# Optimization experiments

Measured on AMD Instinct MI355X. Metric: run time of the kernel, lower is better.

Reference implementation:

```python
import jax, jax.numpy as jnp
import numpy as np

NEG = -1e9


def _siglu(x):
    return x * jax.nn.sigmoid(x)


def setup_inputs() -> dict:
    key = jax.random.key(0)
    ks = jax.random.split(key, 10)
    B, S, M, D = 2, 2048, 64, 1024
    sc = 0.02
    return {
        "tokens": jax.random.normal(ks[0], (B, S, D), jnp.float32),
        "memory": jax.random.normal(ks[1], (B, M, D), jnp.float32),
        "Wq": jax.random.normal(ks[2], (D, D), jnp.float32) * sc,
        "bq": jnp.zeros((D,), jnp.float32),
        "Wk": jax.random.normal(ks[3], (D, D), jnp.float32) * sc,
        "bk": jnp.zeros((D,), jnp.float32),
        "Wv": jax.random.normal(ks[4], (D, D), jnp.float32) * sc,
        "bv": jnp.zeros((D,), jnp.float32),
        "Wo": jax.random.normal(ks[5], (D, D), jnp.float32) * sc,
        "bo": jnp.zeros((D,), jnp.float32),
        "pool_q": jax.random.normal(ks[6], (M, D), jnp.float32),
        "cell_W": jax.random.normal(ks[7], (2 * D, 2 * D), jnp.float32) * sc,
        "cell_b": jnp.zeros((2 * D,), jnp.float32),
    }


def reference(tokens, memory, Wq, bq, Wk, bk, Wv, bv, Wo, bo, pool_q, cell_W, cell_b):
    B, S, D = tokens.shape
    M = memory.shape[1]
    H = 16
    hd = D // H
    T = M + S

    x = jnp.concatenate([memory, tokens], axis=1)  # (B, T, D)

    # combined causal mask: memory rows/cols fully visible, token block causal
    tok_mask = jnp.triu(jnp.full((S, S), NEG, jnp.float32), k=1)
    mask = jnp.zeros((T, T), jnp.float32).at[M:, M:].set(tok_mask)  # (T, T)

    def heads(w, b):
        return (x @ w.T + b).reshape(B, T, H, hd).transpose(0, 2, 1, 3)

    q = heads(Wq, bq)  # (B, H, T, hd)
    k = heads(Wk, bk)
    v = heads(Wv, bv)

    scores = jnp.einsum("bhqd,bhkd->bhqk", q, k) * (hd ** -0.5) + mask
    attn = jax.nn.softmax(scores, axis=-1)
    ctx = jnp.einsum("bhqk,bhkd->bhqd", attn, v)
    ctx = ctx.transpose(0, 2, 1, 3).reshape(B, T, D)
    attn_out = ctx @ Wo.T + bo

    x = x + attn_out  # residual
    mem_out = x[:, :M]  # (B, M, D)
    tok_out = x[:, M:]  # (B, S, D)

    # attention pooling: one learnable query per memory slot
    pscores = jnp.einsum("md,bsd->bms", pool_q, tok_out) * (D ** -0.5)
    pweights = jax.nn.softmax(pscores, axis=-1)
    summary = jnp.einsum("bms,bsd->bmd", pweights, tok_out)  # (B, M, D)

    # MinimalRNNCell (siglu-gated) applied per memory slot
    combined = jnp.concatenate([mem_out, summary], axis=-1)  # (B, M, 2D)
    update = combined @ cell_W.T + cell_b
    gate, cand = jnp.split(update, 2, axis=-1)
    gate = jax.nn.sigmoid(gate)
    new_memory = mem_out * gate + (1.0 - gate) * _siglu(cand)

    return tok_out, new_memory
```

## Files before the change

### kernel.cpp

```cpp
#include <hip/hip_runtime.h>
#include <hip/hip_bf16.h>

#define B_  2
#define S_  2048
#define M_  64
#define D_  1024
#define T_  2112
#define H_  16
#define HD_ 64
#define BT_ (B_*T_)
#define NEGBIG (-1e9f)
#define LOG2E 1.44269504f

typedef float f32x4  __attribute__((ext_vector_type(4)));
typedef float f32x4b __attribute__((ext_vector_type(4)));
typedef short short8 __attribute__((ext_vector_type(8)));
typedef unsigned short u16x4 __attribute__((ext_vector_type(4)));
typedef __bf16 bf16x8 __attribute__((ext_vector_type(8)));

static __device__ __forceinline__ unsigned short bf16_of(float f) {
  __hip_bfloat16 h = __float2bfloat16(f);
  return __builtin_bit_cast(unsigned short, h);
}

static __device__ __forceinline__ f32x4 mfma_bf16(short8 a, short8 b, f32x4 c) {
  return __builtin_amdgcn_mfma_f32_16x16x32_bf16(
      __builtin_bit_cast(bf16x8, a), __builtin_bit_cast(bf16x8, b), c, 0, 0, 0);
}

static __device__ __forceinline__ void gload16(const void* g, void* lds) {
  __builtin_amdgcn_global_load_lds(
      (const __attribute__((address_space(1))) unsigned int*)g,
      (__attribute__((address_space(3))) unsigned int*)lds, 16, 0, 0);
}

static __device__ __forceinline__ short8 pack8(const float* v, float scale) {
  short8 o;
#pragma unroll
  for (int k = 0; k < 8; k++) o[k] = (short)bf16_of(v[k] * scale);
  return o;
}


__global__ void k_build_x(const float* __restrict__ tokens,
                          const float* __restrict__ memory,
                          unsigned short* __restrict__ xb) {
  const int NG = BT_ * D_ / 8;
  for (int gI = blockIdx.x * blockDim.x + threadIdx.x; gI < NG;
       gI += gridDim.x * blockDim.x) {
    int i = gI * 8;
    int b = (i >= T_ * D_) ? 1 : 0;
    int rem = i - b * (T_ * D_);
    int t = rem >> 10;
    int d = rem & 1023;
    const float* src = (t < M_) ? &memory[(((size_t)b * M_ + t) << 10) + d]
                                : &tokens[(((size_t)b * S_ + (t - M_)) << 10) + d];
    float v[8];
    *(f32x4*)&v[0] = *(const f32x4*)&src[0];
    *(f32x4*)&v[4] = *(const f32x4*)&src[4];
    *(short8*)&xb[i] = pack8(v, 1.f);
  }
}

__global__ void k_cast_all(const float* __restrict__ Wq, const float* __restrict__ Wk,
                           const float* __restrict__ Wv, const float* __restrict__ Wo,
                           const float* __restrict__ cW, const float* __restrict__ pq,
                           unsigned short* __restrict__ Wqkvb, unsigned short* __restrict__ Wob,
                           unsigned short* __restrict__ cWb, unsigned short* __restrict__ pqb) {
  const int NW = D_ * D_;
  const int NC = 4 * D_ * D_;
  const int NP = M_ * D_;
  const int NG = (4 * NW + NC + NP) / 8;
  for (int gI = blockIdx.x * blockDim.x + threadIdx.x; gI < NG;
       gI += gridDim.x * blockDim.x) {
    int i = gI * 8;
    const float* src;
    unsigned short* dst;
    float scale = 1.f;
    if (i < 3 * NW) {
      int which = i >> 20, j = i & (NW - 1);
      src = ((which == 0) ? Wq : (which == 1) ? Wk : Wv) + j;
      dst = Wqkvb + i;
    } else if (i < 4 * NW) {
      src = Wo + (i - 3 * NW);
      dst = Wob + (i - 3 * NW);
    } else if (i < 4 * NW + NC) {
      src = cW + (i - 4 * NW);
      dst = cWb + (i - 4 * NW);
    } else {
      src = pq + (i - 4 * NW - NC);
      dst = pqb + (i - 4 * NW - NC);
      scale = 0.03125f * LOG2E;
    }
    float v[8];
    *(f32x4*)&v[0] = *(const f32x4*)&src[0];
    *(f32x4*)&v[4] = *(const f32x4*)&src[4];
    *(short8*)dst = pack8(v, scale);
  }
}

__device__ __forceinline__ void gemm128_core(const unsigned short* __restrict__ A,
                                             const unsigned short* __restrict__ BT,
                                             int K, int m0, int n0,
                                             f32x4 acc[4][4]) {
  __shared__ __align__(16) unsigned short As[2][128][64];
  __shared__ __align__(16) unsigned short Bs[2][128][64];
  const int tid = threadIdx.x;
  const int w = tid >> 6, l = tid & 63;
  const int wr = w >> 1, wc = w & 1;
  const int lr = l & 15, lg = l >> 4;
  f32x4 z; z[0] = z[1] = z[2] = z[3] = 0.f;
#pragma unroll
  for (int i = 0; i < 4; i++)
#pragma unroll
    for (int j = 0; j < 4; j++) acc[i][j] = z;

  auto stage = [&](int buf, int k0) {
#pragma unroll
    for (int c = 0; c < 4; c++) {
      int rbase = c * 32 + w * 8;
      int rr = rbase + (l >> 3);
      int u = (l & 7) ^ (rr & 7);
      gload16(&A[(size_t)(m0 + rr) * K + k0 + u * 8], &As[buf][rbase][0]);
      gload16(&BT[(size_t)(n0 + rr) * K + k0 + u * 8], &Bs[buf][rbase][0]);
    }
  };

  stage(0, 0);
  int cur = 0;
  const int NK = K >> 6;
  for (int kt = 0; kt < NK; kt++) {
    if (kt + 1 < NK) {
      stage(cur ^ 1, (kt + 1) << 6);
      asm volatile("s_waitcnt vmcnt(8)" ::: "memory");
    } else {
      asm volatile("s_waitcnt vmcnt(0)" ::: "memory");
    }
    __builtin_amdgcn_s_barrier();

    short8 a[4][2], b[4][2];
#pragma unroll
    for (int i = 0; i < 4; i++) {
      int row = wr * 64 + i * 16 + lr;
      int sw = row & 7;
#pragma unroll
      for (int kk = 0; kk < 2; kk++)
        a[i][kk] = *(const short8*)&As[cur][row][(((kk << 2) | lg) ^ sw) * 8];
    }
#pragma unroll
    for (int j = 0; j < 4; j++) {
      int row = wc * 64 + j * 16 + lr;
      int sw = row & 7;
#pragma unroll
      for (int kk = 0; kk < 2; kk++)
        b[j][kk] = *(const short8*)&Bs[cur][row][(((kk << 2) | lg) ^ sw) * 8];
    }
    __builtin_amdgcn_s_setprio(1);
#pragma unroll
    for (int kk = 0; kk < 2; kk++)
#pragma unroll
      for (int i = 0; i < 4; i++)
#pragma unroll
        for (int j = 0; j < 4; j++)
          acc[i][j] = mfma_bf16(a[i][kk], b[j][kk], acc[i][j]);
    __builtin_amdgcn_s_setprio(0);

    __builtin_amdgcn_s_barrier();
    cur ^= 1;
  }
}

__device__ __forceinline__ void gemm_core(const unsigned short* __restrict__ A,
                                          const unsigned short* __restrict__ BT,
                                          int ldk, int Klen, int m0, int n0,
                                          f32x4 acc[4]) {
  __shared__ __align__(16) unsigned short As[64][40];
  __shared__ __align__(16) unsigned short Bs[64][40];
  const int tid = threadIdx.x;
  const int w = tid >> 6, l = tid & 63;
  const int sr = tid >> 2, sc = (tid & 3) * 8;
  f32x4 z; z[0] = z[1] = z[2] = z[3] = 0.f;
  acc[0] = acc[1] = acc[2] = acc[3] = z;
  for (int k0 = 0; k0 < Klen; k0 += 32) {
    __syncthreads();
    *(short8*)&As[sr][sc] = *(const short8*)&A[(size_t)(m0 + sr) * ldk + k0 + sc];
    *(short8*)&Bs[sr][sc] = *(const short8*)&BT[(size_t)(n0 + sr) * ldk + k0 + sc];
    __syncthreads();
    short8 a = *(const short8*)&As[w * 16 + (l & 15)][(l >> 4) * 8];
#pragma unroll
    for (int n = 0; n < 4; n++) {
      short8 b = *(const short8*)&Bs[n * 16 + (l & 15)][(l >> 4) * 8];
      acc[n] = mfma_bf16(a, b, acc[n]);
    }
  }
}

__global__ __launch_bounds__(256) void k_qkv(
    const unsigned short* __restrict__ xb, const unsigned short* __restrict__ Wqkvb,
    const float* __restrict__ bq, const float* __restrict__ bk,
    const float* __restrict__ bv, unsigned short* __restrict__ qg,
    unsigned short* __restrict__ kg, unsigned short* __restrict__ vTg) {
  const int id = blockIdx.x;
  const int xcd = id & 7;
  const int g = xcd * 99 + (id >> 3);
  const int mt = g / 24, nn = g - mt * 24;
  const int which = nn >> 3;
  const unsigned short* W = Wqkvb + (size_t)which * D_ * D_;
  const float* bias = (which == 0) ? bq : ((which == 1) ? bk : bv);
  f32x4 acc[4][4];
  const int m0 = mt * 128, n0 = (nn & 7) * 128;
  gemm128_core(xb, W, D_, m0, n0, acc);
  const int tid = threadIdx.x, w = tid >> 6, l = tid & 63;
  const int wr = w >> 1, wc = w & 1;
#pragma unroll
  for (int i = 0; i < 4; i++) {
#pragma unroll
    for (int j = 0; j < 4; j++) {
#pragma unroll
      for (int r = 0; r < 4; r++) {
        int m = m0 + wr * 64 + i * 16 + (l >> 4) * 4 + r;
        int c = n0 + wc * 64 + j * 16 + (l & 15);
        int b = (m >= T_) ? 1 : 0;
        int t = m - b * T_;
        int h = c >> 6, dh = c & 63;
        int bh = b * H_ + h;
        float v = acc[i][j][r] + bias[c];
        if (which == 0)
          qg[((size_t)bh * T_ + t) * HD_ + dh] = bf16_of(v * 0.125f * LOG2E);
        else if (which == 1)
          kg[((size_t)bh * T_ + t) * HD_ + dh] = bf16_of(v);
        else
          vTg[((size_t)bh * HD_ + dh) * T_ + t] = bf16_of(v);
      }
    }
  }
}

__global__ __launch_bounds__(256) void k_attn(
    const unsigned short* __restrict__ qg, const unsigned short* __restrict__ kg,
    const unsigned short* __restrict__ vTg, unsigned short* __restrict__ ctx) {
  const int id = blockIdx.x;
  const int xcd = id & 7;
  const int rem = id >> 3;
  const int g = rem / 33, qtr = rem - g * 33;
  const int qt = (qtr == 0) ? 0 : 33 - qtr;
  const int bh = g * 8 + xcd;
  const int tid = threadIdx.x, w = tid >> 6, l = tid & 63;
  const int lr = l & 15, lg = l >> 4;
  __shared__ __align__(16) unsigned short Ks[2][64][64];
  __shared__ __align__(16) unsigned short Vs[2][64][64];
  __shared__ __align__(16) unsigned short Ps[4][16][72];

  const unsigned short* qb = qg + (size_t)bh * T_ * HD_;
  const unsigned short* kb = kg + (size_t)bh * T_ * HD_;
  const unsigned short* vb = vTg + (size_t)bh * HD_ * T_;

  short8 aq[2];
  const int qrow = qt * 64 + w * 16 + lr;
#pragma unroll
  for (int st = 0; st < 2; st++)
    aq[st] = *(const short8*)&qb[(size_t)qrow * HD_ + st * 32 + lg * 8];

  f32x4 zz; zz[0] = zz[1] = zz[2] = zz[3] = 0.f;
  f32x4 o[4];
  o[0] = o[1] = o[2] = o[3] = zz;
  float mrun = -1e30f, lrun = 0.f;

  const int nkt = (qt == 0) ? 33 : qt + 1;

  auto stage = [&](int buf, int kb2) {
#pragma unroll
    for (int i = 0; i < 2; i++) {
      int rr = w * 16 + i * 8 + (l >> 3);
      int swz = ((l & 7) ^ (rr & 7)) * 8;
      gload16(&kb[(size_t)(kb2 + rr) * HD_ + swz], &Ks[buf][w * 16 + i * 8][0]);
      gload16(&vb[(size_t)rr * T_ + kb2 + swz], &Vs[buf][w * 16 + i * 8][0]);
    }
  };

  stage(0, 0);
  __syncthreads();
  int cur = 0;

  for (int j = 0; j < nkt; j++) {
    const int kbase = j * 64;
    if (j + 1 < nkt) stage(cur ^ 1, kbase + 64);

    short8 bkf[2][4];
#pragma unroll
    for (int n = 0; n < 4; n++) {
      int row = n * 16 + lr;
      int sw = lr & 7;
#pragma unroll
      for (int st = 0; st < 2; st++)
        bkf[st][n] = *(const short8*)&Ks[cur][row][((st * 4 + lg) ^ sw) * 8];
    }
    f32x4 s[4];
    s[0] = s[1] = s[2] = s[3] = zz;
    __builtin_amdgcn_s_setprio(1);
#pragma unroll
    for (int st = 0; st < 2; st++)
#pragma unroll
      for (int n = 0; n < 4; n++)
        s[n] = mfma_bf16(bkf[st][n], aq[st], s[n]);
    __builtin_amdgcn_s_setprio(0);

    if (qt > 0 && j == qt) {
      const int tql = w * 16 + lr;
#pragma unroll
      for (int n = 0; n < 4; n++)
#pragma unroll
        for (int r = 0; r < 4; r++) {
          int tkl = n * 16 + lg * 4 + r;
          if (tkl > tql) s[n][r] = NEGBIG;
        }
    }
    float pm = s[0][0];
#pragma unroll
    for (int n = 0; n < 4; n++)
#pragma unroll
      for (int r = 0; r < 4; r++) pm = fmaxf(pm, s[n][r]);
    pm = fmaxf(pm, __shfl_xor(pm, 16));
    pm = fmaxf(pm, __shfl_xor(pm, 32));

    if (__any(pm > mrun + 8.f)) {
      float mn = fmaxf(mrun, pm);
      float fac = exp2f(mrun - mn);
      mrun = mn;
      lrun *= fac;
      float fr[4];
#pragma unroll
      for (int r = 0; r < 4; r++) fr[r] = __shfl(fac, lg * 4 + r);
#pragma unroll
      for (int n = 0; n < 4; n++)
#pragma unroll
        for (int r = 0; r < 4; r++) o[n][r] *= fr[r];
    }
#pragma unroll
    for (int n = 0; n < 4; n++) {
      u16x4 pk;
#pragma unroll
      for (int r = 0; r < 4; r++) {
        float p = exp2f(s[n][r] - mrun);
        lrun += p;
        pk[r] = bf16_of(p);
      }
      *(u16x4*)&Ps[w][lr][n * 16 + lg * 4] = pk;
    }

    short8 bvf[2][4];
#pragma unroll
    for (int n = 0; n < 4; n++) {
      int row = n * 16 + lr;
      int sw = lr & 7;
#pragma unroll
      for (int st = 0; st < 2; st++)
        bvf[st][n] = *(const short8*)&Vs[cur][row][((st * 4 + lg) ^ sw) * 8];
    }
    short8 ap[2];
#pragma unroll
    for (int st = 0; st < 2; st++)
      ap[st] = *(const short8*)&Ps[w][lr][st * 32 + lg * 8];
    __builtin_amdgcn_s_setprio(1);
#pragma unroll
    for (int st = 0; st < 2; st++)
#pragma unroll
      for (int n = 0; n < 4; n++)
        o[n] = mfma_bf16(ap[st], bvf[st][n], o[n]);
    __builtin_amdgcn_s_setprio(0);

    __syncthreads();
    cur ^= 1;
  }
  lrun += __shfl_xor(lrun, 16);
  lrun += __shfl_xor(lrun, 32);
  float linv[4];
#pragma unroll
  for (int r = 0; r < 4; r++) linv[r] = 1.f / __shfl(lrun, lg * 4 + r);

  const int b = bh >> 4, h = bh & 15;
#pragma unroll
  for (int n = 0; n < 4; n++)
#pragma unroll
    for (int r = 0; r < 4; r++) {
      int tq = qt * 64 + w * 16 + lg * 4 + r;
      float val = o[n][r] * linv[r];
      ctx[((size_t)(b * T_ + tq)) * D_ + h * HD_ + n * 16 + lr] = bf16_of(val);
    }
}

__global__ __launch_bounds__(256) void k_out(
    const unsigned short* __restrict__ ctxb, const unsigned short* __restrict__ Wob,
    const float* __restrict__ bo, const float* __restrict__ tokens,
    const float* __restrict__ memory, float* __restrict__ out_tok,
    unsigned short* __restrict__ tokb, unsigned short* __restrict__ tokTb,
    float* __restrict__ memout, unsigned short* __restrict__ comb) {
  f32x4 acc[4][4];
  const int m0 = blockIdx.y * 128, n0 = blockIdx.x * 128;
  gemm128_core(ctxb, Wob, D_, m0, n0, acc);
  const int tid = threadIdx.x, w = tid >> 6, l = tid & 63;
  const int wr = w >> 1, wc = w & 1;
#pragma unroll
  for (int i = 0; i < 4; i++) {
#pragma unroll
    for (int j = 0; j < 4; j++) {
#pragma unroll
      for (int r = 0; r < 4; r++) {
        int m = m0 + wr * 64 + i * 16 + (l >> 4) * 4 + r;
        int c = n0 + wc * 64 + j * 16 + (l & 15);
        int b = (m >= T_) ? 1 : 0;
        int t = m - b * T_;
        float xo = (t < M_) ? memory[((size_t)b * M_ + t) * D_ + c]
                            : tokens[((size_t)b * S_ + (t - M_)) * D_ + c];
        float val = acc[i][j][r] + bo[c] + xo;
        if (t < M_) {
          memout[((size_t)b * M_ + t) * D_ + c] = val;
          comb[((size_t)b * M_ + t) * (2 * D_) + c] = bf16_of(val);
        } else {
          size_t ti = (size_t)b * S_ + (t - M_);
          out_tok[ti * D_ + c] = val;
          tokb[ti * D_ + c] = bf16_of(val);
          tokTb[((size_t)b * D_ + c) * S_ + (t - M_)] = bf16_of(val);
        }
      }
    }
  }
}

__global__ __launch_bounds__(256) void k_pscore_part(
    const unsigned short* __restrict__ pqb, const unsigned short* __restrict__ tokb,
    float* __restrict__ pscp) {
  const int stile = blockIdx.x, ks = blockIdx.y, b = blockIdx.z;
  f32x4 acc[4];
  gemm_core(pqb + ks * 256, tokb + (size_t)b * S_ * D_ + ks * 256, D_, 256,
            0, stile * 64, acc);
  const int tid = threadIdx.x, w = tid >> 6, l = tid & 63;
  float* dst = pscp + ((size_t)(ks * B_ + b) * M_) * S_;
#pragma unroll
  for (int n = 0; n < 4; n++) {
#pragma unroll
    for (int r = 0; r < 4; r++) {
      int m = w * 16 + (l >> 4) * 4 + r;
      int s = stile * 64 + n * 16 + (l & 15);
      dst[(size_t)m * S_ + s] = acc[n][r];
    }
  }
}

__global__ __launch_bounds__(256) void k_psoftmax(const float* __restrict__ pscp,
                                                  unsigned short* __restrict__ pw) {
  const int row = blockIdx.x;
  const int b = row >> 6, m = row & 63;
  const int tid = threadIdx.x;
  float v[8];
  float mx = -1e30f;
#pragma unroll
  for (int i = 0; i < 8; i++) {
    int s = tid + i * 256;
    float acc = 0.f;
#pragma unroll
    for (int ks = 0; ks < 4; ks++)
      acc += pscp[((size_t)(ks * B_ + b) * M_ + m) * S_ + s];
    v[i] = acc;
    mx = fmaxf(mx, acc);
  }
#pragma unroll
  for (int off = 1; off < 64; off <<= 1) mx = fmaxf(mx, __shfl_xor(mx, off));
  __shared__ float rm[4], rs[4];
  if ((tid & 63) == 0) rm[tid >> 6] = mx;
  __syncthreads();
  mx = fmaxf(fmaxf(rm[0], rm[1]), fmaxf(rm[2], rm[3]));
  float sum = 0.f;
#pragma unroll
  for (int i = 0; i < 8; i++) {
    v[i] = exp2f(v[i] - mx);
    sum += v[i];
  }
#pragma unroll
  for (int off = 1; off < 64; off <<= 1) sum += __shfl_xor(sum, off);
  if ((tid & 63) == 0) rs[tid >> 6] = sum;
  __syncthreads();
  float inv = 1.f / (rs[0] + rs[1] + rs[2] + rs[3]);
#pragma unroll
  for (int i = 0; i < 8; i++)
    pw[(size_t)row * S_ + tid + i * 256] = bf16_of(v[i] * inv);
}

__global__ __launch_bounds__(256) void k_summary_part(
    const unsigned short* __restrict__ pw, const unsigned short* __restrict__ tokTb,
    float* __restrict__ sump) {
  const int nt = blockIdx.x, ks = blockIdx.y, b = blockIdx.z;
  f32x4 acc[4];
  gemm_core(pw + (size_t)b * M_ * S_ + ks * 256,
            tokTb + (size_t)b * D_ * S_ + ks * 256, S_, 256, 0, nt * 64, acc);
  const int tid = threadIdx.x, w = tid >> 6, l = tid & 63;
  float* dst = sump + ((size_t)(ks * B_ + b) * M_) * D_;
#pragma unroll
  for (int n = 0; n < 4; n++) {
#pragma unroll
    for (int r = 0; r < 4; r++) {
      int m = w * 16 + (l >> 4) * 4 + r;
      int c = nt * 64 + n * 16 + (l & 15);
      dst[(size_t)m * D_ + c] = acc[n][r];
    }
  }
}

__global__ void k_sumcomb(const float* __restrict__ sump,
                          unsigned short* __restrict__ comb) {
  int i = blockIdx.x * blockDim.x + threadIdx.x;
  if (i >= B_ * M_ * D_) return;
  int bm = i >> 10, c = i & 1023;
  int b = bm >> 6, m = bm & 63;
  float acc = 0.f;
#pragma unroll
  for (int ks = 0; ks < 8; ks++)
    acc += sump[((size_t)(ks * B_ + b) * M_ + m) * D_ + c];
  comb[((size_t)b * M_ + m) * (2 * D_) + D_ + c] = bf16_of(acc);
}

__global__ __launch_bounds__(256) void k_cell_part(
    const unsigned short* __restrict__ comb, const unsigned short* __restrict__ cWb,
    float* __restrict__ cellp) {
  const int nt = blockIdx.x, mt = blockIdx.y, ks = blockIdx.z;
  f32x4 acc[4];
  gemm_core(comb + ks * 512, cWb + ks * 512, 2 * D_, 512, mt * 64, nt * 64, acc);
  const int tid = threadIdx.x, w = tid >> 6, l = tid & 63;
#pragma unroll
  for (int n = 0; n < 4; n++) {
#pragma unroll
    for (int r = 0; r < 4; r++) {
      int m = mt * 64 + w * 16 + (l >> 4) * 4 + r;
      int c = nt * 64 + n * 16 + (l & 15);
      cellp[((size_t)ks * (B_ * M_) + m) * (2 * D_) + c] = acc[n][r];
    }
  }
}

__global__ void k_newmem(const float* __restrict__ cellp,
                         const float* __restrict__ cb,
                         const float* __restrict__ memout,
                         float* __restrict__ out2) {
  int i = blockIdx.x * blockDim.x + threadIdx.x;
  if (i >= B_ * M_ * D_) return;
  int r = i >> 10, d = i & 1023;
  float gsum = cb[d], csum = cb[D_ + d];
#pragma unroll
  for (int ks = 0; ks < 4; ks++) {
    gsum += cellp[((size_t)ks * (B_ * M_) + r) * (2 * D_) + d];
    csum += cellp[((size_t)ks * (B_ * M_) + r) * (2 * D_) + D_ + d];
  }
  float sg = 1.f / (1.f + __expf(-gsum));
  float sc = 1.f / (1.f + __expf(-csum));
  out2[i] = memout[i] * sg + (1.f - sg) * (csum * sc);
}

extern "C" void kernel_launch(void* const* d_in, const int* in_sizes, int n_in,
                              void* d_out, int out_size, void* d_ws, size_t ws_size,
                              hipStream_t stream) {
  const float* tokens = (const float*)d_in[0];
  const float* memory = (const float*)d_in[1];
  const float* Wq = (const float*)d_in[2];
  const float* bq = (const float*)d_in[3];
  const float* Wk = (const float*)d_in[4];
  const float* bk = (const float*)d_in[5];
  const float* Wv = (const float*)d_in[6];
  const float* bv = (const float*)d_in[7];
  const float* Wo = (const float*)d_in[8];
  const float* bo = (const float*)d_in[9];
  const float* pool_q = (const float*)d_in[10];
  const float* cell_W = (const float*)d_in[11];
  const float* cell_b = (const float*)d_in[12];

  size_t off = 0;
  auto alloc = [&](size_t bytes) -> void* {
    void* p = (char*)d_ws + off;
    off += (bytes + 255) & ~(size_t)255;
    return p;
  };
  unsigned short* xb    = (unsigned short*)alloc((size_t)BT_ * D_ * 2);
  unsigned short* Wqkvb = (unsigned short*)alloc((size_t)3 * D_ * D_ * 2);
  unsigned short* Wob   = (unsigned short*)alloc((size_t)D_ * D_ * 2);
  unsigned short* cWb   = (unsigned short*)alloc((size_t)(2 * D_) * (2 * D_) * 2);
  unsigned short* pqb   = (unsigned short*)alloc((size_t)M_ * D_ * 2);
  unsigned short* qg    = (unsigned short*)alloc((size_t)B_ * H_ * T_ * HD_ * 2);
  unsigned short* kg    = (unsigned short*)alloc((size_t)B_ * H_ * T_ * HD_ * 2);
  unsigned short* vTg   = (unsigned short*)alloc((size_t)B_ * H_ * HD_ * T_ * 2);
  unsigned short* ctxb  = (unsigned short*)alloc((size_t)BT_ * D_ * 2);
  unsigned short* tokb  = (unsigned short*)alloc((size_t)B_ * S_ * D_ * 2);
  unsigned short* tokTb = (unsigned short*)alloc((size_t)B_ * D_ * S_ * 2);
  float*          memout= (float*)alloc((size_t)B_ * M_ * D_ * 4);
  unsigned short* comb  = (unsigned short*)alloc((size_t)B_ * M_ * 2 * D_ * 2);
  unsigned short* pwt   = (unsigned short*)alloc((size_t)B_ * M_ * S_ * 2);
  float*          pscp  = (float*)alloc((size_t)4 * B_ * M_ * S_ * 4);
  float*          sump  = (float*)alloc((size_t)8 * B_ * M_ * D_ * 4);
  float*          cellp = (float*)alloc((size_t)4 * B_ * M_ * 2 * D_ * 4);

  float* out_tok = (float*)d_out;
  float* out_mem = out_tok + (size_t)B_ * S_ * D_;

  k_build_x<<<2048, 256, 0, stream>>>(tokens, memory, xb);
  k_cast_all<<<2048, 256, 0, stream>>>(Wq, Wk, Wv, Wo, cell_W, pool_q,
                                       Wqkvb, Wob, cWb, pqb);

  k_qkv<<<792, 256, 0, stream>>>(xb, Wqkvb, bq, bk, bv, qg, kg, vTg);
  k_attn<<<1056, 256, 0, stream>>>(qg, kg, vTg, ctxb);
  k_out<<<dim3(8, 33), 256, 0, stream>>>(ctxb, Wob, bo, tokens, memory, out_tok,
                                         tokb, tokTb, memout, comb);
  k_pscore_part<<<dim3(32, 4, 2), 256, 0, stream>>>(pqb, tokb, pscp);
  k_psoftmax<<<B_ * M_, 256, 0, stream>>>(pscp, pwt);
  k_summary_part<<<dim3(16, 8, 2), 256, 0, stream>>>(pwt, tokTb, sump);
  k_sumcomb<<<512, 256, 0, stream>>>(sump, comb);
  k_cell_part<<<dim3(32, 2, 4), 256, 0, stream>>>(comb, cWb, cellp);
  k_newmem<<<512, 256, 0, stream>>>(cellp, cell_b, memout, out_mem);
}
```

Baseline: 220.6 us.

## Merge prep kernels, drop XCD block remap, halve split-K factors

Fuses the activation build and weight-cast kernels into one k_prep launch to save a launch and a tail. Replaces k_qkv's XCD-aware block index remapping with a plain 2D grid. Halves the split-K partition count for the pooling-score, summary and cell GEMMs, which reduces partial-sum traffic and reduction work but lowers parallelism for these small GEMMs.

New measurement: 235.7 us. 6.8% more time.

```diff
diff --git a/kernel.cpp b/kernel.cpp
--- a/kernel.cpp
+++ b/kernel.cpp
@@ -13,7 +13,6 @@
 #define LOG2E 1.44269504f
 
 typedef float f32x4  __attribute__((ext_vector_type(4)));
-typedef float f32x4b __attribute__((ext_vector_type(4)));
 typedef short short8 __attribute__((ext_vector_type(8)));
 typedef unsigned short u16x4 __attribute__((ext_vector_type(4)));
 typedef __bf16 bf16x8 __attribute__((ext_vector_type(8)));
@@ -41,56 +40,49 @@
   return o;
 }
 
-
-__global__ void k_build_x(const float* __restrict__ tokens,
-                          const float* __restrict__ memory,
-                          unsigned short* __restrict__ xb) {
-  const int NG = BT_ * D_ / 8;
-  for (int gI = blockIdx.x * blockDim.x + threadIdx.x; gI < NG;
-       gI += gridDim.x * blockDim.x) {
-    int i = gI * 8;
-    int b = (i >= T_ * D_) ? 1 : 0;
-    int rem = i - b * (T_ * D_);
-    int t = rem >> 10;
-    int d = rem & 1023;
-    const float* src = (t < M_) ? &memory[(((size_t)b * M_ + t) << 10) + d]
-                                : &tokens[(((size_t)b * S_ + (t - M_)) << 10) + d];
-    float v[8];
-    *(f32x4*)&v[0] = *(const f32x4*)&src[0];
-    *(f32x4*)&v[4] = *(const f32x4*)&src[4];
-    *(short8*)&xb[i] = pack8(v, 1.f);
-  }
-}
-
-__global__ void k_cast_all(const float* __restrict__ Wq, const float* __restrict__ Wk,
-                           const float* __restrict__ Wv, const float* __restrict__ Wo,
-                           const float* __restrict__ cW, const float* __restrict__ pq,
-                           unsigned short* __restrict__ Wqkvb, unsigned short* __restrict__ Wob,
-                           unsigned short* __restrict__ cWb, unsigned short* __restrict__ pqb) {
+__global__ void k_prep(const float* __restrict__ tokens, const float* __restrict__ memory,
+                       const float* __restrict__ Wq, const float* __restrict__ Wk,
+                       const float* __restrict__ Wv, const float* __restrict__ Wo,
+                       const float* __restrict__ cW, const float* __restrict__ pq,
+                       unsigned short* __restrict__ xb, unsigned short* __restrict__ Wqkvb,
+                       unsigned short* __restrict__ Wob, unsigned short* __restrict__ cWb,
+                       unsigned short* __restrict__ pqb) {
   const int NW = D_ * D_;
   const int NC = 4 * D_ * D_;
   const int NP = M_ * D_;
-  const int NG = (4 * NW + NC + NP) / 8;
+  const int NG1 = BT_ * D_ / 8;
+  const int NG = NG1 + (4 * NW + NC + NP) / 8;
   for (int gI = blockIdx.x * blockDim.x + threadIdx.x; gI < NG;
        gI += gridDim.x * blockDim.x) {
-    int i = gI * 8;
     const float* src;
     unsigned short* dst;
     float scale = 1.f;
-    if (i < 3 * NW) {
-      int which = i >> 20, j = i & (NW - 1);
-      src = ((which == 0) ? Wq : (which == 1) ? Wk : Wv) + j;
-      dst = Wqkvb + i;
-    } else if (i < 4 * NW) {
-      src = Wo + (i - 3 * NW);
-      dst = Wob + (i - 3 * NW);
-    } else if (i < 4 * NW + NC) {
-      src = cW + (i - 4 * NW);
-      dst = cWb + (i - 4 * NW);
+    if (gI < NG1) {
+      int i = gI * 8;
+      int b = (i >= T_ * D_) ? 1 : 0;
+      int rem = i - b * (T_ * D_);
+      int t = rem >> 10;
+      int d = rem & 1023;
+      src = (t < M_) ? &memory[(((size_t)b * M_ + t) << 10) + d]
+                     : &tokens[(((size_t)b * S_ + (t - M_)) << 10) + d];
+      dst = xb + i;
     } else {
-      src = pq + (i - 4 * NW - NC);
-      dst = pqb + (i - 4 * NW - NC);
-      scale = 0.03125f * LOG2E;
+      int i = (gI - NG1) * 8;
+      if (i < 3 * NW) {
+        int which = i >> 20, j = i & (NW - 1);
+        src = ((which == 0) ? Wq : (which == 1) ? Wk : Wv) + j;
+        dst = Wqkvb + i;
+      } else if (i < 4 * NW) {
+        src = Wo + (i - 3 * NW);
+        dst = Wob + (i - 3 * NW);
+      } else if (i < 4 * NW + NC) {
+        src = cW + (i - 4 * NW);
+        dst = cWb + (i - 4 * NW);
+      } else {
+        src = pq + (i - 4 * NW - NC);
+        dst = pqb + (i - 4 * NW - NC);
+        scale = 0.03125f * LOG2E;
+      }
     }
     float v[8];
     *(f32x4*)&v[0] = *(const f32x4*)&src[0];
@@ -200,15 +192,11 @@
     const float* __restrict__ bq, const float* __restrict__ bk,
     const float* __restrict__ bv, unsigned short* __restrict__ qg,
     unsigned short* __restrict__ kg, unsigned short* __restrict__ vTg) {
-  const int id = blockIdx.x;
-  const int xcd = id & 7;
-  const int g = xcd * 99 + (id >> 3);
-  const int mt = g / 24, nn = g - mt * 24;
-  const int which = nn >> 3;
+  const int which = blockIdx.x >> 3;
   const unsigned short* W = Wqkvb + (size_t)which * D_ * D_;
   const float* bias = (which == 0) ? bq : ((which == 1) ? bk : bv);
   f32x4 acc[4][4];
-  const int m0 = mt * 128, n0 = (nn & 7) * 128;
+  const int m0 = blockIdx.y * 128, n0 = (blockIdx.x & 7) * 128;
   gemm128_core(xb, W, D_, m0, n0, acc);
   const int tid = threadIdx.x, w = tid >> 6, l = tid & 63;
   const int wr = w >> 1, wc = w & 1;
@@ -432,7 +420,7 @@
     float* __restrict__ pscp) {
   const int stile = blockIdx.x, ks = blockIdx.y, b = blockIdx.z;
   f32x4 acc[4];
-  gemm_core(pqb + ks * 256, tokb + (size_t)b * S_ * D_ + ks * 256, D_, 256,
+  gemm_core(pqb + ks * 512, tokb + (size_t)b * S_ * D_ + ks * 512, D_, 512,
             0, stile * 64, acc);
   const int tid = threadIdx.x, w = tid >> 6, l = tid & 63;
   float* dst = pscp + ((size_t)(ks * B_ + b) * M_) * S_;
@@ -459,7 +447,7 @@
     int s = tid + i * 256;
     float acc = 0.f;
 #pragma unroll
-    for (int ks = 0; ks < 4; ks++)
+    for (int ks = 0; ks < 2; ks++)
       acc += pscp[((size_t)(ks * B_ + b) * M_ + m) * S_ + s];
     v[i] = acc;
     mx = fmaxf(mx, acc);
@@ -491,8 +479,8 @@
     float* __restrict__ sump) {
   const int nt = blockIdx.x, ks = blockIdx.y, b = blockIdx.z;
   f32x4 acc[4];
-  gemm_core(pw + (size_t)b * M_ * S_ + ks * 256,
-            tokTb + (size_t)b * D_ * S_ + ks * 256, S_, 256, 0, nt * 64, acc);
+  gemm_core(pw + (size_t)b * M_ * S_ + ks * 512,
+            tokTb + (size_t)b * D_ * S_ + ks * 512, S_, 512, 0, nt * 64, acc);
   const int tid = threadIdx.x, w = tid >> 6, l = tid & 63;
   float* dst = sump + ((size_t)(ks * B_ + b) * M_) * D_;
 #pragma unroll
@@ -514,7 +502,7 @@
   int b = bm >> 6, m = bm & 63;
   float acc = 0.f;
 #pragma unroll
-  for (int ks = 0; ks < 8; ks++)
+  for (int ks = 0; ks < 4; ks++)
     acc += sump[((size_t)(ks * B_ + b) * M_ + m) * D_ + c];
   comb[((size_t)b * M_ + m) * (2 * D_) + D_ + c] = bf16_of(acc);
 }
@@ -524,7 +512,7 @@
     float* __restrict__ cellp) {
   const int nt = blockIdx.x, mt = blockIdx.y, ks = blockIdx.z;
   f32x4 acc[4];
-  gemm_core(comb + ks * 512, cWb + ks * 512, 2 * D_, 512, mt * 64, nt * 64, acc);
+  gemm_core(comb + ks * 1024, cWb + ks * 1024, 2 * D_, 1024, mt * 64, nt * 64, acc);
   const int tid = threadIdx.x, w = tid >> 6, l = tid & 63;
 #pragma unroll
   for (int n = 0; n < 4; n++) {
@@ -546,7 +534,7 @@
   int r = i >> 10, d = i & 1023;
   float gsum = cb[d], csum = cb[D_ + d];
 #pragma unroll
-  for (int ks = 0; ks < 4; ks++) {
+  for (int ks = 0; ks < 2; ks++) {
     gsum += cellp[((size_t)ks * (B_ * M_) + r) * (2 * D_) + d];
     csum += cellp[((size_t)ks * (B_ * M_) + r) * (2 * D_) + D_ + d];
   }
@@ -592,25 +580,24 @@
   float*          memout= (float*)alloc((size_t)B_ * M_ * D_ * 4);
   unsigned short* comb  = (unsigned short*)alloc((size_t)B_ * M_ * 2 * D_ * 2);
   unsigned short* pwt   = (unsigned short*)alloc((size_t)B_ * M_ * S_ * 2);
-  float*          pscp  = (float*)alloc((size_t)4 * B_ * M_ * S_ * 4);
-  float*          sump  = (float*)alloc((size_t)8 * B_ * M_ * D_ * 4);
-  float*          cellp = (float*)alloc((size_t)4 * B_ * M_ * 2 * D_ * 4);
+  float*          pscp  = (float*)alloc((size_t)2 * B_ * M_ * S_ * 4);
+  float*          sump  = (float*)alloc((size_t)4 * B_ * M_ * D_ * 4);
+  float*          cellp = (float*)alloc((size_t)2 * B_ * M_ * 2 * D_ * 4);
 
   float* out_tok = (float*)d_out;
   float* out_mem = out_tok + (size_t)B_ * S_ * D_;
 
-  k_build_x<<<2048, 256, 0, stream>>>(tokens, memory, xb);
-  k_cast_all<<<2048, 256, 0, stream>>>(Wq, Wk, Wv, Wo, cell_W, pool_q,
-                                       Wqkvb, Wob, cWb, pqb);
-
-  k_qkv<<<792, 256, 0, stream>>>(xb, Wqkvb, bq, bk, bv, qg, kg, vTg);
+  k_prep<<<2048, 256, 0, stream>>>(tokens, memory, Wq, Wk, Wv, Wo, cell_W, pool_q,
+                                   xb, Wqkvb, Wob, cWb, pqb);
+
+  k_qkv<<<dim3(24, 33), 256, 0, stream>>>(xb, Wqkvb, bq, bk, bv, qg, kg, vTg);
   k_attn<<<1056, 256, 0, stream>>>(qg, kg, vTg, ctxb);
   k_out<<<dim3(8, 33), 256, 0, stream>>>(ctxb, Wob, bo, tokens, memory, out_tok,
                                          tokb, tokTb, memout, comb);
-  k_pscore_part<<<dim3(32, 4, 2), 256, 0, stream>>>(pqb, tokb, pscp);
+  k_pscore_part<<<dim3(32, 2, 2), 256, 0, stream>>>(pqb, tokb, pscp);
   k_psoftmax<<<B_ * M_, 256, 0, stream>>>(pscp, pwt);
-  k_summary_part<<<dim3(16, 8, 2), 256, 0, stream>>>(pwt, tokTb, sump);
+  k_summary_part<<<dim3(16, 4, 2), 256, 0, stream>>>(pwt, tokTb, sump);
   k_sumcomb<<<512, 256, 0, stream>>>(sump, comb);
-  k_cell_part<<<dim3(32, 2, 4), 256, 0, stream>>>(comb, cWb, cellp);
+  k_cell_part<<<dim3(32, 2, 2), 256, 0, stream>>>(comb, cWb, cellp);
   k_newmem<<<512, 256, 0, stream>>>(cellp, cell_b, memout, out_mem);
 }
```
